# Optimization experiments

Measured on AMD Instinct MI355X. Metric: run time of the kernel, lower is better.

Reference implementation:

```python
import jax, jax.numpy as jnp
import numpy as np

TQ, TK, H, HEADS = 2048, 2048, 1024, 16

def setup_inputs() -> dict:
    key = jax.random.key(0)
    ks = jax.random.split(key, 11)
    s = 1.0 / np.sqrt(H).astype(np.float32)
    return {
        "Q": jax.random.normal(ks[0], (TQ, H), jnp.float32),
        "K": jax.random.normal(ks[1], (TK, H), jnp.float32),
        "V": jax.random.normal(ks[2], (TK, H), jnp.float32),
        "Wq": jax.random.normal(ks[3], (H, H), jnp.float32) * s,
        "bq": jax.random.normal(ks[4], (H,), jnp.float32) * s,
        "Wk": jax.random.normal(ks[5], (H, H), jnp.float32) * s,
        "bk": jax.random.normal(ks[6], (H,), jnp.float32) * s,
        "Wv": jax.random.normal(ks[7], (H, H), jnp.float32) * s,
        "bv": jax.random.normal(ks[8], (H,), jnp.float32) * s,
        # linear_out: nn.Linear(num_heads, 1) -> weight [num_heads], bias scalar
        "Wo": jax.random.normal(ks[9], (HEADS,), jnp.float32) / np.sqrt(HEADS).astype(np.float32),
        "bo": jax.random.normal(ks[10], (), jnp.float32) / np.sqrt(HEADS).astype(np.float32),
    }

def reference(Q, K, V, Wq, bq, Wk, bk, Wv, bv, Wo, bo):
    heads = Wo.shape[0]
    # relu(linear) projections
    Q_l = jax.nn.relu(Q @ Wq.T + bq)            # [Tq, H]
    K_l = jax.nn.relu(K @ Wk.T + bk)            # [Tk, H]
    V_l = jax.nn.relu(V @ Wv.T + bv)            # [Tk, H]
    Tq, Hd = Q_l.shape
    Tk = K_l.shape[0]
    d = Hd // heads                              # head dim
    Qh = Q_l.reshape(Tq, heads, d)               # split heads (torch split+cat over dim0)
    Kh = K_l.reshape(Tk, heads, d)
    # per-head scaled scores: [Tq, Tk, heads]
    scale = np.float32(1.0 / np.sqrt(d))
    scores = jnp.einsum('qhd,khd->qkh', Qh, Kh) * scale
    # learned linear combine over heads -> [Tq, Tk]
    logits = scores @ Wo + bo
    attn = jax.nn.softmax(logits, axis=1)        # softmax over Tk
    out = attn @ V_l                             # [Tq, H]
    return out, attn.T                           # attention.transpose(1,0) -> [Tk, Tq]
```

## Files before the change

### kernel.cpp

```cpp
#include <hip/hip_runtime.h>
#include <stdint.h>


#define TQ 2048
#define TK 2048
#define HD 1024

#define DEVI __device__ __forceinline__

typedef __attribute__((ext_vector_type(8))) short bf16x8;
typedef __attribute__((ext_vector_type(4))) float f32x4;
typedef __attribute__((ext_vector_type(4))) unsigned short u16x4;

DEVI unsigned short f2bf(float f) {
  uint32_t u = __builtin_bit_cast(uint32_t, f);
  u += 0x7FFFu + ((u >> 16) & 1u);
  return (unsigned short)(u >> 16);
}
DEVI float bf2f(unsigned short h) {
  uint32_t u = ((uint32_t)h) << 16;
  return __builtin_bit_cast(float, u);
}
DEVI void gload_lds16(const void* g, void* l) {
  __builtin_amdgcn_global_load_lds((const __attribute__((address_space(1))) void*)g,
                                   (__attribute__((address_space(3))) void*)l,
                                   16, 0, 0);
}
template<int N> DEVI void wait_vm() { asm volatile("s_waitcnt vmcnt(%0)" :: "n"(N) : "memory"); }
DEVI void wait_lgkm0() { asm volatile("s_waitcnt lgkmcnt(0)" ::: "memory"); }
#define SBAR() __builtin_amdgcn_s_barrier()

DEVI void stageT(const unsigned short* __restrict__ A, const unsigned short* __restrict__ B,
                 int lda, int ldb, int k0, unsigned short* buf, int tid) {
#pragma unroll
  for (int i = 0; i < 2; i++) {
    int c = i * 512 + tid;
    int r = c >> 3;
    int cs = (c & 7) ^ (r & 7);
    gload_lds16(A + (size_t)r * lda + k0 + cs * 8, buf + c * 8);
  }
#pragma unroll
  for (int i = 0; i < 2; i++) {
    int c = i * 512 + tid;
    int r = c >> 3;
    int cs = (c & 7) ^ (r & 7);
    gload_lds16(B + (size_t)r * ldb + k0 + cs * 8, buf + 8192 + c * 8);
  }
}

DEVI void computeT(const unsigned short* lA, const unsigned short* lB, f32x4 (*acc)[2],
                   int wr, int wc, int l15, int hi) {
#pragma unroll
  for (int kk = 0; kk < 2; kk++) {
    bf16x8 af[4], bfr[2];
#pragma unroll
    for (int f = 0; f < 4; f++) {
      int ra = wr * 64 + f * 16 + l15;
      int ca = (kk * 4 + hi) ^ (ra & 7);
      af[f] = *(const bf16x8*)(lA + ra * 64 + ca * 8);
    }
#pragma unroll
    for (int f = 0; f < 2; f++) {
      int rb = wc * 32 + f * 16 + l15;
      int cb = (kk * 4 + hi) ^ (rb & 7);
      bfr[f] = *(const bf16x8*)(lB + rb * 64 + cb * 8);
    }
#pragma unroll
    for (int fm = 0; fm < 4; fm++)
#pragma unroll
      for (int fn = 0; fn < 2; fn++)
        acc[fm][fn] = __builtin_amdgcn_mfma_f32_16x16x32_bf16(af[fm], bfr[fn], acc[fm][fn], 0, 0, 0);
  }
}

template<int NKT>
DEVI void mfma_pipeline(const unsigned short* __restrict__ A, const unsigned short* __restrict__ B,
                        int lda, int ldb, unsigned short* lds, f32x4 (*acc)[2]) {
  constexpr int LPS = 4;
  constexpr int BSTR = 16384;
  const int tid = threadIdx.x;
  const int lane = tid & 63, wave = tid >> 6;
  const int l15 = lane & 15, hi = lane >> 4;
  const int wr = wave >> 2, wc = wave & 3;

#pragma unroll
  for (int i = 0; i < 4; i++)
#pragma unroll
    for (int j = 0; j < 2; j++) acc[i][j] = (f32x4)(0.0f);

#pragma unroll
  for (int s = 0; s < 3; s++) stageT(A, B, lda, ldb, s * 64, lds + s * BSTR, tid);

#pragma unroll 1
  for (int t = 0; t < NKT; ++t) {
    if (t < NKT - 2) wait_vm<2 * LPS>();
    else if (t == NKT - 2) wait_vm<LPS>();
    else wait_vm<0>();
    SBAR();
    unsigned short* buf = lds + (t & 3) * BSTR;
    __builtin_amdgcn_s_setprio(1);
    computeT(buf, buf + 8192, acc, wr, wc, l15, hi);
    __builtin_amdgcn_s_setprio(0);
    wait_lgkm0();
    if (t + 3 < NKT) stageT(A, B, lda, ldb, (t + 3) * 64, lds + ((t + 3) & 3) * BSTR, tid);
  }
}

__global__ __launch_bounds__(512)
void gemm_proj(const unsigned short* __restrict__ Qb, const unsigned short* __restrict__ Kb,
               const unsigned short* __restrict__ Vb,
               const unsigned short* __restrict__ Wqb, const unsigned short* __restrict__ Wkb,
               const unsigned short* __restrict__ Wvb,
               const float* __restrict__ bq, const float* __restrict__ bk,
               const float* __restrict__ bv, const float* __restrict__ Wo,
               unsigned short* __restrict__ Ql, unsigned short* __restrict__ Ks,
               unsigned short* __restrict__ VT) {
  __shared__ __align__(16) unsigned short lds[4 * 16384];
  const int bid = blockIdx.x;
  const int x = bid & 7, j = bid >> 3;
  const int z = j >> 4;
  const int jj = j & 15;
  const int bm = (x & 3) * 4 + (jj >> 2);
  const int bn = (x >> 2) * 4 + (jj & 3);

  const unsigned short* A = (z == 0) ? Qb : (z == 1) ? Kb : Vb;
  const unsigned short* B = (z == 0) ? Wqb : (z == 1) ? Wkb : Wvb;
  const float* bias = (z == 0) ? bq : (z == 1) ? bk : bv;

  f32x4 acc[4][2];
  mfma_pipeline<16>(A + (size_t)bm * 128 * HD, B + (size_t)bn * 128 * HD, HD, HD, lds, acc);

  const int tid = threadIdx.x;
  const int lane = tid & 63, wave = tid >> 6;
  const int wr = wave >> 2, wc = wave & 3;
  const int l15 = lane & 15, hi = lane >> 4;
  const int row0 = bm * 128 + wr * 64;
  const int col0 = bn * 128 + wc * 32;

#pragma unroll
  for (int fm = 0; fm < 4; fm++)
#pragma unroll
    for (int fn = 0; fn < 2; fn++) {
      int cg = col0 + fn * 16 + l15;
      int rg = row0 + fm * 16 + hi * 4;
      float b = bias[cg];
      if (z == 2) {
        u16x4 o;
#pragma unroll
        for (int i = 0; i < 4; i++) o[i] = f2bf(fmaxf(acc[fm][fn][i] + b, 0.0f));
        *(u16x4*)(VT + (size_t)cg * TK + rg) = o;
      } else if (z == 1) {
        float s = 0.125f * Wo[cg >> 6];
#pragma unroll
        for (int i = 0; i < 4; i++)
          Ks[(size_t)(rg + i) * HD + cg] = f2bf(fmaxf(acc[fm][fn][i] + b, 0.0f) * s);
      } else {
#pragma unroll
        for (int i = 0; i < 4; i++)
          Ql[(size_t)(rg + i) * HD + cg] = f2bf(fmaxf(acc[fm][fn][i] + b, 0.0f));
      }
    }
}

__global__ __launch_bounds__(512)
void gemm_logits(const unsigned short* __restrict__ Ql, const unsigned short* __restrict__ Ks,
                 float* __restrict__ C) {
  __shared__ __align__(16) unsigned short lds[4 * 16384];
  const int bid = blockIdx.x;
  const int x = bid & 7, j = bid >> 3;
  const int bm = (x & 3) * 4 + (j >> 3);
  const int bn = (x >> 2) * 8 + (j & 7);

  f32x4 acc[4][2];
  mfma_pipeline<16>(Ql + (size_t)bm * 128 * HD, Ks + (size_t)bn * 128 * HD, HD, HD, lds, acc);

  const int tid = threadIdx.x;
  const int lane = tid & 63, wave = tid >> 6;
  const int wr = wave >> 2, wc = wave & 3;
  const int l15 = lane & 15, hi = lane >> 4;
  const int row0 = bm * 128 + wr * 64;
  const int col0 = bn * 128 + wc * 32;
#pragma unroll
  for (int fm = 0; fm < 4; fm++)
#pragma unroll
    for (int fn = 0; fn < 2; fn++) {
      int cg = col0 + fn * 16 + l15;
      int rg = row0 + fm * 16 + hi * 4;
#pragma unroll
      for (int i = 0; i < 4; i++)
        C[(size_t)(rg + i) * TK + cg] = acc[fm][fn][i];
    }
}

__global__ __launch_bounds__(512)
void pv_and_transpose(const unsigned short* __restrict__ attnb, const unsigned short* __restrict__ VT,
                      float* __restrict__ outp, float* __restrict__ attnT) {
  __shared__ __align__(16) unsigned short lds[4 * 16384];
  const int bid = blockIdx.x;
  const int tid = threadIdx.x;
  if (bid < 128) {
    const int x = bid & 7, j = bid >> 3;
    const int bm = (x & 3) * 4 + (j >> 2);
    const int bn = (x >> 2) * 4 + (j & 3);
    f32x4 acc[4][2];
    mfma_pipeline<32>(attnb + (size_t)bm * 128 * TK, VT + (size_t)bn * 128 * TK,
                      TK, TK, lds, acc);
    const int lane = tid & 63, wave = tid >> 6;
    const int wr = wave >> 2, wc = wave & 3;
    const int l15 = lane & 15, hi = lane >> 4;
    const int row0 = bm * 128 + wr * 64;
    const int col0 = bn * 128 + wc * 32;
#pragma unroll
    for (int fm = 0; fm < 4; fm++)
#pragma unroll
      for (int fn = 0; fn < 2; fn++) {
        int cg = col0 + fn * 16 + l15;
        int rg = row0 + fm * 16 + hi * 4;
#pragma unroll
        for (int i = 0; i < 4; i++)
          outp[(size_t)(rg + i) * HD + cg] = acc[fm][fn][i];
      }
  } else {
    unsigned short (*tile)[68] = reinterpret_cast<unsigned short (*)[68]>(lds);
    const int q0 = bid - 128;
    const int tr = (q0 >> 5) * 64;
    const int tc = (q0 & 31) * 64;
#pragma unroll
    for (int i = 0; i < 2; i++) {
      int q = i * 512 + tid;
      int r = q >> 4;
      int c4 = (q & 15) * 4;
      u16x4 v = *(const u16x4*)(attnb + (size_t)(tr + r) * TK + tc + c4);
      *(u16x4*)(&tile[r][c4]) = v;
    }
    __syncthreads();
#pragma unroll
    for (int i = 0; i < 2; i++) {
      int q = i * 512 + tid;
      int c = q >> 4;
      int r4 = (q & 15) * 4;
      f32x4 o;
#pragma unroll
      for (int jx = 0; jx < 4; jx++) o[jx] = bf2f(tile[r4 + jx][c]);
      *(f32x4*)(attnT + (size_t)(tc + c) * TQ + tr + r4) = o;
    }
  }
}

__global__ __launch_bounds__(256)
void softmax_k(const float* __restrict__ logits, unsigned short* __restrict__ attnb) {
  const int row = blockIdx.x;
  const int tid = threadIdx.x;
  const int lane = tid & 63;
  const int wave = tid >> 6;
  const float* lr = logits + (size_t)row * TK;

  f32x4 v0 = *(const f32x4*)(lr + tid * 8);
  f32x4 v1 = *(const f32x4*)(lr + tid * 8 + 4);
  float x[8];
#pragma unroll
  for (int j = 0; j < 4; j++) { x[j] = v0[j]; x[4 + j] = v1[j]; }

  float m = x[0];
#pragma unroll
  for (int j = 1; j < 8; j++) m = fmaxf(m, x[j]);
  for (int o = 32; o > 0; o >>= 1) m = fmaxf(m, __shfl_xor(m, o));
  __shared__ float redm[4], reds[4];
  if (lane == 0) redm[wave] = m;
  __syncthreads();
  m = fmaxf(fmaxf(redm[0], redm[1]), fmaxf(redm[2], redm[3]));

  const float L2E = 1.44269504088896341f;
  float e[8];
  float s = 0.0f;
#pragma unroll
  for (int j = 0; j < 8; j++) { e[j] = exp2f((x[j] - m) * L2E); s += e[j]; }
  for (int o = 32; o > 0; o >>= 1) s += __shfl_xor(s, o);
  if (lane == 0) reds[wave] = s;
  __syncthreads();
  s = reds[0] + reds[1] + reds[2] + reds[3];
  float inv = 1.0f / s;

  unsigned short* ar = attnb + (size_t)row * TK;
  u16x4 o0, o1;
#pragma unroll
  for (int j = 0; j < 4; j++) { o0[j] = f2bf(e[j] * inv); o1[j] = f2bf(e[4 + j] * inv); }
  *(u16x4*)(ar + tid * 8) = o0;
  *(u16x4*)(ar + tid * 8 + 4) = o1;
}

__global__ __launch_bounds__(256)
void cvt6(const float* __restrict__ Q, const float* __restrict__ K, const float* __restrict__ V,
          const float* __restrict__ Wq, const float* __restrict__ Wk, const float* __restrict__ Wv,
          unsigned short* __restrict__ Qb, unsigned short* __restrict__ Kb,
          unsigned short* __restrict__ Vb, unsigned short* __restrict__ Wqb,
          unsigned short* __restrict__ Wkb, unsigned short* __restrict__ Wvb) {
  const int y = blockIdx.y;
  const float* s;
  unsigned short* d;
  int n4;
  switch (y) {
    case 0: s = Q;  d = Qb;  n4 = TQ * HD / 4; break;
    case 1: s = K;  d = Kb;  n4 = TK * HD / 4; break;
    case 2: s = V;  d = Vb;  n4 = TK * HD / 4; break;
    case 3: s = Wq; d = Wqb; n4 = HD * HD / 4; break;
    case 4: s = Wk; d = Wkb; n4 = HD * HD / 4; break;
    default: s = Wv; d = Wvb; n4 = HD * HD / 4; break;
  }
  int i = blockIdx.x * 256 + threadIdx.x;
  if (i < n4) {
    f32x4 v = *(const f32x4*)(s + i * 4);
    u16x4 o;
#pragma unroll
    for (int j = 0; j < 4; j++) o[j] = f2bf(v[j]);
    *(u16x4*)(d + i * 4) = o;
  }
}

extern "C" void kernel_launch(void* const* d_in, const int* in_sizes, int n_in,
                              void* d_out, int out_size, void* d_ws, size_t ws_size,
                              hipStream_t stream) {
  const float* Q  = (const float*)d_in[0];
  const float* K  = (const float*)d_in[1];
  const float* V  = (const float*)d_in[2];
  const float* Wq = (const float*)d_in[3];
  const float* bq = (const float*)d_in[4];
  const float* Wk = (const float*)d_in[5];
  const float* bk = (const float*)d_in[6];
  const float* Wv = (const float*)d_in[7];
  const float* bv = (const float*)d_in[8];
  const float* Wo = (const float*)d_in[9];

  uint8_t* w = (uint8_t*)d_ws;
  unsigned short* Qb  = (unsigned short*)(w + 0);
  unsigned short* Kb  = (unsigned short*)(w + 4194304);
  unsigned short* Vb  = (unsigned short*)(w + 8388608);
  unsigned short* Wqb = (unsigned short*)(w + 12582912);
  unsigned short* Wkb = (unsigned short*)(w + 14680064);
  unsigned short* Wvb = (unsigned short*)(w + 16777216);
  unsigned short* Ql  = (unsigned short*)(w + 18874368);
  unsigned short* Ks  = (unsigned short*)(w + 23068672);
  unsigned short* VT  = (unsigned short*)(w + 27262976);
  float*          logits = (float*)(w + 31457280);
  unsigned short* attnb  = (unsigned short*)(w + 48234496);

  float* outp  = (float*)d_out;
  float* attnT = outp + (size_t)TQ * HD;

  cvt6<<<dim3(2048, 6), dim3(256), 0, stream>>>(Q, K, V, Wq, Wk, Wv, Qb, Kb, Vb, Wqb, Wkb, Wvb);

  gemm_proj<<<dim3(384), dim3(512), 0, stream>>>(Qb, Kb, Vb, Wqb, Wkb, Wvb,
                                                 bq, bk, bv, Wo, Ql, Ks, VT);

  gemm_logits<<<dim3(256), dim3(512), 0, stream>>>(Ql, Ks, logits);

  softmax_k<<<dim3(TQ), dim3(256), 0, stream>>>(logits, attnb);

  pv_and_transpose<<<dim3(1152), dim3(512), 0, stream>>>(attnb, VT, outp, attnT);
}
```

Before: 76.32 us.

## Switch GEMM pipeline to double buffering and stage V transpose through LDS

The shared MFMA pipeline drops from a 4-slot, 3-deep LDS ring to a 2-slot double buffer and adds an extra barrier before refilling the slot just consumed. LDS per block halves and launch bounds now request 4 blocks per CU, so more blocks can be resident at once. The projection kernel gets a new block-to-tile mapping, and its V output is first transposed in LDS and then written to VT with coalesced stores instead of scattered ones. The cost is a shallower prefetch plus an extra barrier per k-step, which exposes more global-load latency.

```diff
diff --git a/kernel.cpp b/kernel.cpp
--- a/kernel.cpp
+++ b/kernel.cpp
@@ -76,8 +76,6 @@
 template<int NKT>
 DEVI void mfma_pipeline(const unsigned short* __restrict__ A, const unsigned short* __restrict__ B,
                         int lda, int ldb, unsigned short* lds, f32x4 (*acc)[2]) {
-  constexpr int LPS = 4;
-  constexpr int BSTR = 16384;
   const int tid = threadIdx.x;
   const int lane = tid & 63, wave = tid >> 6;
   const int l15 = lane & 15, hi = lane >> 4;
@@ -88,25 +86,25 @@
 #pragma unroll
     for (int j = 0; j < 2; j++) acc[i][j] = (f32x4)(0.0f);
 
-#pragma unroll
-  for (int s = 0; s < 3; s++) stageT(A, B, lda, ldb, s * 64, lds + s * BSTR, tid);
+  stageT(A, B, lda, ldb, 0, lds, tid);
+  stageT(A, B, lda, ldb, 64, lds + 16384, tid);
 
 #pragma unroll 1
   for (int t = 0; t < NKT; ++t) {
-    if (t < NKT - 2) wait_vm<2 * LPS>();
-    else if (t == NKT - 2) wait_vm<LPS>();
+    if (t < NKT - 1) wait_vm<4>();
     else wait_vm<0>();
     SBAR();
-    unsigned short* buf = lds + (t & 3) * BSTR;
+    unsigned short* buf = lds + (t & 1) * 16384;
     __builtin_amdgcn_s_setprio(1);
     computeT(buf, buf + 8192, acc, wr, wc, l15, hi);
     __builtin_amdgcn_s_setprio(0);
     wait_lgkm0();
-    if (t + 3 < NKT) stageT(A, B, lda, ldb, (t + 3) * 64, lds + ((t + 3) & 3) * BSTR, tid);
-  }
-}
-
-__global__ __launch_bounds__(512)
+    SBAR();
+    if (t + 2 < NKT) stageT(A, B, lda, ldb, (t + 2) * 64, buf, tid);
+  }
+}
+
+__global__ __launch_bounds__(512, 4)
 void gemm_proj(const unsigned short* __restrict__ Qb, const unsigned short* __restrict__ Kb,
                const unsigned short* __restrict__ Vb,
                const unsigned short* __restrict__ Wqb, const unsigned short* __restrict__ Wkb,
@@ -115,13 +113,13 @@
                const float* __restrict__ bv, const float* __restrict__ Wo,
                unsigned short* __restrict__ Ql, unsigned short* __restrict__ Ks,
                unsigned short* __restrict__ VT) {
-  __shared__ __align__(16) unsigned short lds[4 * 16384];
+  __shared__ __align__(16) unsigned short lds[2 * 16384];
   const int bid = blockIdx.x;
   const int x = bid & 7, j = bid >> 3;
-  const int z = j >> 4;
-  const int jj = j & 15;
-  const int bm = (x & 3) * 4 + (jj >> 2);
-  const int bn = (x >> 2) * 4 + (jj & 3);
+  const int bmz = x * 6 + (j >> 3);
+  const int bn = j & 7;
+  const int z = bmz >> 4;
+  const int bm = bmz & 15;
 
   const unsigned short* A = (z == 0) ? Qb : (z == 1) ? Kb : Vb;
   const unsigned short* B = (z == 0) ? Wqb : (z == 1) ? Wkb : Wvb;
@@ -137,35 +135,53 @@
   const int row0 = bm * 128 + wr * 64;
   const int col0 = bn * 128 + wc * 32;
 
-#pragma unroll
-  for (int fm = 0; fm < 4; fm++)
-#pragma unroll
-    for (int fn = 0; fn < 2; fn++) {
-      int cg = col0 + fn * 16 + l15;
-      int rg = row0 + fm * 16 + hi * 4;
-      float b = bias[cg];
-      if (z == 2) {
-        u16x4 o;
-#pragma unroll
-        for (int i = 0; i < 4; i++) o[i] = f2bf(fmaxf(acc[fm][fn][i] + b, 0.0f));
-        *(u16x4*)(VT + (size_t)cg * TK + rg) = o;
-      } else if (z == 1) {
-        float s = 0.125f * Wo[cg >> 6];
+  if (z == 2) {
+    unsigned short (*T)[132] = reinterpret_cast<unsigned short (*)[132]>(lds);
+#pragma unroll
+    for (int fm = 0; fm < 4; fm++)
+#pragma unroll
+      for (int fn = 0; fn < 2; fn++) {
+        int cl = wc * 32 + fn * 16 + l15;
+        float b = bias[bn * 128 + cl];
 #pragma unroll
         for (int i = 0; i < 4; i++)
-          Ks[(size_t)(rg + i) * HD + cg] = f2bf(fmaxf(acc[fm][fn][i] + b, 0.0f) * s);
-      } else {
-#pragma unroll
-        for (int i = 0; i < 4; i++)
-          Ql[(size_t)(rg + i) * HD + cg] = f2bf(fmaxf(acc[fm][fn][i] + b, 0.0f));
+          T[cl][wr * 64 + fm * 16 + hi * 4 + i] = f2bf(fmaxf(acc[fm][fn][i] + b, 0.0f));
       }
-    }
-}
-
-__global__ __launch_bounds__(512)
+    __syncthreads();
+#pragma unroll
+    for (int i = 0; i < 8; i++) {
+      int h = i * 512 + tid;
+      int c = h >> 5;
+      int rq = h & 31;
+      u16x4 v = *(const u16x4*)(&T[c][rq * 4]);
+      *(u16x4*)(VT + (size_t)(bn * 128 + c) * TK + bm * 128 + rq * 4) = v;
+    }
+  } else {
+#pragma unroll
+    for (int fm = 0; fm < 4; fm++)
+#pragma unroll
+      for (int fn = 0; fn < 2; fn++) {
+        int cg = col0 + fn * 16 + l15;
+        int rg = row0 + fm * 16 + hi * 4;
+        float b = bias[cg];
+        if (z == 1) {
+          float s = 0.125f * Wo[cg >> 6];
+#pragma unroll
+          for (int i = 0; i < 4; i++)
+            Ks[(size_t)(rg + i) * HD + cg] = f2bf(fmaxf(acc[fm][fn][i] + b, 0.0f) * s);
+        } else {
+#pragma unroll
+          for (int i = 0; i < 4; i++)
+            Ql[(size_t)(rg + i) * HD + cg] = f2bf(fmaxf(acc[fm][fn][i] + b, 0.0f));
+        }
+      }
+  }
+}
+
+__global__ __launch_bounds__(512, 4)
 void gemm_logits(const unsigned short* __restrict__ Ql, const unsigned short* __restrict__ Ks,
                  float* __restrict__ C) {
-  __shared__ __align__(16) unsigned short lds[4 * 16384];
+  __shared__ __align__(16) unsigned short lds[2 * 16384];
   const int bid = blockIdx.x;
   const int x = bid & 7, j = bid >> 3;
   const int bm = (x & 3) * 4 + (j >> 3);
@@ -192,10 +208,10 @@
     }
 }
 
-__global__ __launch_bounds__(512)
+__global__ __launch_bounds__(512, 4)
 void pv_and_transpose(const unsigned short* __restrict__ attnb, const unsigned short* __restrict__ VT,
                       float* __restrict__ outp, float* __restrict__ attnT) {
-  __shared__ __align__(16) unsigned short lds[4 * 16384];
+  __shared__ __align__(16) unsigned short lds[2 * 16384];
   const int bid = blockIdx.x;
   const int tid = threadIdx.x;
   if (bid < 128) {
```

Result: faster. 74.01 us (-3.0%).
